# Performance work log

Measured on AMD Instinct MI355X. Metric: run time of the kernel, lower is better.

Reference implementation:

```python
import jax, jax.numpy as jnp
import numpy as np

N_NODES = 50000
N_EDGES = 800000
IN_CH, HIDDEN, OUT_CH = 128, 128, 64
EPS = 1e-5


def setup_inputs() -> dict:
    key = jax.random.key(0)
    ks = jax.random.split(key, 16)
    s = lambda fan_in: 1.0 / np.sqrt(fan_in)
    return {
        "x": jax.random.normal(ks[0], (N_NODES, IN_CH), dtype=jnp.float32),
        "edge_index": jax.random.randint(ks[1], (2, N_EDGES), 0, N_NODES, dtype=jnp.int64),
        # SAGEConv1: lin_l (neighbors, with bias), lin_r (root, no bias)
        "Wl1": jax.random.uniform(ks[2], (HIDDEN, IN_CH), jnp.float32, -s(IN_CH), s(IN_CH)),
        "bl1": jnp.zeros((HIDDEN,), jnp.float32),
        "Wr1": jax.random.uniform(ks[3], (HIDDEN, IN_CH), jnp.float32, -s(IN_CH), s(IN_CH)),
        # SAGEConv2
        "Wl2": jax.random.uniform(ks[4], (HIDDEN, HIDDEN), jnp.float32, -s(HIDDEN), s(HIDDEN)),
        "bl2": jnp.zeros((HIDDEN,), jnp.float32),
        "Wr2": jax.random.uniform(ks[5], (HIDDEN, HIDDEN), jnp.float32, -s(HIDDEN), s(HIDDEN)),
        # SAGEConv3
        "Wl3": jax.random.uniform(ks[6], (OUT_CH, HIDDEN), jnp.float32, -s(HIDDEN), s(HIDDEN)),
        "bl3": jnp.zeros((OUT_CH,), jnp.float32),
        "Wr3": jax.random.uniform(ks[7], (OUT_CH, HIDDEN), jnp.float32, -s(HIDDEN), s(HIDDEN)),
        # LayerNorms
        "g1": jnp.ones((HIDDEN,), jnp.float32),
        "beta1": jnp.zeros((HIDDEN,), jnp.float32),
        "g2": jnp.ones((HIDDEN,), jnp.float32),
        "beta2": jnp.zeros((HIDDEN,), jnp.float32),
    }


def _sage_conv(x, src, dst, n_nodes, Wl, bl, Wr):
    # mean aggregation of source features at target nodes (PyG SAGEConv, aggr='mean')
    msg = x[src]                                             # [E, C] gather
    sums = jax.ops.segment_sum(msg, dst, num_segments=n_nodes)
    cnt = jax.ops.segment_sum(jnp.ones((src.shape[0],), x.dtype), dst, num_segments=n_nodes)
    mean = sums / jnp.maximum(cnt, 1.0)[:, None]
    return mean @ Wl.T + bl + x @ Wr.T


def _layernorm(h, g, b):
    mu = jnp.mean(h, axis=-1, keepdims=True)
    var = jnp.mean(jnp.square(h - mu), axis=-1, keepdims=True)
    return (h - mu) * jax.lax.rsqrt(var + EPS) * g + b


def reference(x, edge_index, Wl1, bl1, Wr1, Wl2, bl2, Wr2, Wl3, bl3, Wr3, g1, beta1, g2, beta2):
    src, dst = edge_index[0], edge_index[1]
    n = x.shape[0]
    h = jax.nn.relu(_sage_conv(x, src, dst, n, Wl1, bl1, Wr1))
    h = _layernorm(h, g1, beta1)
    h = jax.nn.relu(_sage_conv(h, src, dst, n, Wl2, bl2, Wr2))
    h = _layernorm(h, g2, beta2)
    return _sage_conv(h, src, dst, n, Wl3, bl3, Wr3)
```

## Files before the change

kernel.cpp:

```cpp
#include <hip/hip_runtime.h>

#define NNODES 50000
#define NEDGES 800000
#define FILL_CHUNK 7168
#define FILL_NCHUNK 112
#define FILL_BLOCKS (FILL_NCHUNK * 8)
#define GEMM_BLOCKS ((NNODES + 127) / 128)
#define FUSE_BLOCKS ((NNODES + 127) / 128)
#define CAP 64
#define HSTRIDE 136

using bf16x8  = __attribute__((ext_vector_type(8))) __bf16;
using floatx4 = __attribute__((ext_vector_type(4))) float;

__device__ __forceinline__ float bf2f(unsigned short u) {
  unsigned int v = ((unsigned int)u) << 16;
  return __builtin_bit_cast(float, v);
}
__device__ __forceinline__ unsigned short f2bf(float f) {
  unsigned int u = __builtin_bit_cast(unsigned int, f);
  u += 0x7fffu + ((u >> 16) & 1u);
  return (unsigned short)(u >> 16);
}

__device__ __forceinline__ signed char enc_i8(float f) {
  float g = fminf(fmaxf(f * 32.0f, -127.0f), 127.0f);
  return (signed char)__float2int_rn(g);
}

struct WPtrs {
  const float* src[6];
  unsigned short* dst[6];
  int n[6];
};

__global__ __launch_bounds__(256) void convw_zero_kernel(WPtrs p, int* __restrict__ cnt) {
  if (blockIdx.x < 320) {
    int i = blockIdx.x * 256 + threadIdx.x;
#pragma unroll
    for (int s = 0; s < 6; ++s) {
      if (i < p.n[s]) {
        p.dst[s][i] = f2bf(p.src[s][i]);
        return;
      }
      i -= p.n[s];
    }
  } else {
    int i = (blockIdx.x - 320) * 256 + threadIdx.x;
    if (i < NNODES) cnt[i] = 0;
  }
}

__device__ __forceinline__ void fill_body(int bid, const int* __restrict__ src,
                                          const int* __restrict__ dst,
                                          int* __restrict__ cnt,
                                          int* __restrict__ bucket) {
  int p = bid & 7;
  if (p == 7) return;
  int chunk = bid >> 3;
  int e0 = chunk * FILL_CHUNK;
  int e1 = min(e0 + FILL_CHUNK, NEDGES);
  for (int base = e0 + (int)threadIdx.x * 4; base < e1; base += 256 * 4) {
    int4 d4 = *(const int4*)(dst + base);
    int4 s4 = *(const int4*)(src + base);
    if ((d4.x >> 13) == p) { int sl = atomicAdd(&cnt[d4.x], 1); if (sl < CAP) bucket[(size_t)d4.x * CAP + sl] = s4.x; }
    if ((d4.y >> 13) == p) { int sl = atomicAdd(&cnt[d4.y], 1); if (sl < CAP) bucket[(size_t)d4.y * CAP + sl] = s4.y; }
    if ((d4.z >> 13) == p) { int sl = atomicAdd(&cnt[d4.z], 1); if (sl < CAP) bucket[(size_t)d4.z * CAP + sl] = s4.z; }
    if ((d4.w >> 13) == p) { int sl = atomicAdd(&cnt[d4.w], 1); if (sl < CAP) bucket[(size_t)d4.w * CAP + sl] = s4.w; }
  }
}

__device__ __forceinline__ bf16x8 load_frag(const unsigned short* p) {
  uint4 v = *(const uint4*)p;
  return __builtin_bit_cast(bf16x8, v);
}
__device__ __forceinline__ bf16x8 cvt_frag(const float* p) {
  float4 v0 = *(const float4*)p;
  float4 v1 = *(const float4*)(p + 4);
  uint4 o;
  o.x = (unsigned int)f2bf(v0.x) | ((unsigned int)f2bf(v0.y) << 16);
  o.y = (unsigned int)f2bf(v0.z) | ((unsigned int)f2bf(v0.w) << 16);
  o.z = (unsigned int)f2bf(v1.x) | ((unsigned int)f2bf(v1.y) << 16);
  o.w = (unsigned int)f2bf(v1.z) | ((unsigned int)f2bf(v1.w) << 16);
  return __builtin_bit_cast(bf16x8, o);
}

template <int NTL, int NTR, bool F32IN>
__device__ __forceinline__ void gemm_dual_body(int bid, const void* __restrict__ Ain,
                                               const unsigned short* __restrict__ W,
                                               signed char* __restrict__ yl,
                                               unsigned short* __restrict__ yr) {
  constexpr int NT = NTL + NTR;
  int wave = threadIdx.x >> 6;
  int lane = threadIdx.x & 63;
  int quad = lane >> 4;
  int m = lane & 15;
  int row0 = bid * 128 + wave * 32;
  int ar0 = min(row0 + m, NNODES - 1);
  int ar1 = min(row0 + 16 + m, NNODES - 1);
  bf16x8 a0[4], a1[4];
#pragma unroll
  for (int kt = 0; kt < 4; ++kt) {
    if constexpr (F32IN) {
      const float* A = (const float*)Ain;
      a0[kt] = cvt_frag(A + (size_t)ar0 * 128 + quad * 8 + kt * 32);
      a1[kt] = cvt_frag(A + (size_t)ar1 * 128 + quad * 8 + kt * 32);
    } else {
      const unsigned short* A = (const unsigned short*)Ain;
      a0[kt] = load_frag(A + (size_t)ar0 * 128 + quad * 8 + kt * 32);
      a1[kt] = load_frag(A + (size_t)ar1 * 128 + quad * 8 + kt * 32);
    }
  }
#pragma unroll
  for (int t = 0; t < NT; ++t) {
    const unsigned short* wp = W + (t * 16 + m) * 128 + quad * 8;
    bf16x8 w[4];
#pragma unroll
    for (int kt = 0; kt < 4; ++kt) w[kt] = load_frag(wp + kt * 32);
    floatx4 c0 = {0.f, 0.f, 0.f, 0.f};
    floatx4 c1 = {0.f, 0.f, 0.f, 0.f};
#pragma unroll
    for (int kt = 0; kt < 4; ++kt) {
      c0 = __builtin_amdgcn_mfma_f32_16x16x32_bf16(a0[kt], w[kt], c0, 0, 0, 0);
      c1 = __builtin_amdgcn_mfma_f32_16x16x32_bf16(a1[kt], w[kt], c1, 0, 0, 0);
    }
#pragma unroll
    for (int r = 0; r < 4; ++r) {
      int g0 = row0 + quad * 4 + r;
      int g1r = g0 + 16;
      if (t < NTL) {
        int col = t * 16 + m;
        if (g0 < NNODES) yl[(size_t)g0 * (NTL * 16) + col] = enc_i8(c0[r]);
        if (g1r < NNODES) yl[(size_t)g1r * (NTL * 16) + col] = enc_i8(c1[r]);
      } else {
        int col = (t - NTL) * 16 + m;
        if (g0 < NNODES) yr[(size_t)g0 * (NTR * 16) + col] = f2bf(c0[r]);
        if (g1r < NNODES) yr[(size_t)g1r * (NTR * 16) + col] = f2bf(c1[r]);
      }
    }
  }
}

__global__ __launch_bounds__(256) void fill_gemm1_kernel(
    const int* __restrict__ src, const int* __restrict__ dst, int* __restrict__ cnt,
    int* __restrict__ bucket, const float* __restrict__ x,
    const unsigned short* __restrict__ W, signed char* __restrict__ yl,
    unsigned short* __restrict__ yr) {
  if (blockIdx.x < FILL_BLOCKS)
    fill_body(blockIdx.x, src, dst, cnt, bucket);
  else
    gemm_dual_body<8, 8, true>(blockIdx.x - FILL_BLOCKS, x, W, yl, yr);
}

#define ACCU(u, base)                                       \
  a[base] += (int)((signed char)((u) & 0xffu));             \
  a[base + 1] += (int)((signed char)(((u) >> 8) & 0xffu));  \
  a[base + 2] += (int)((signed char)(((u) >> 16) & 0xffu)); \
  a[base + 3] += (int)((signed char)((u) >> 24));
#define ACC16(v) ACCU((v).x, 0) ACCU((v).y, 4) ACCU((v).z, 8) ACCU((v).w, 12)

template <int NTL, int NTR>
__global__ __launch_bounds__(1024) void aggln_gemm_kernel(
    const signed char* __restrict__ yl_in, const unsigned short* __restrict__ yr_in,
    const float* __restrict__ bl, const float* __restrict__ g,
    const float* __restrict__ be, const int* __restrict__ cnt,
    const int* __restrict__ bucket, const unsigned short* __restrict__ W,
    signed char* __restrict__ yl_out, unsigned short* __restrict__ yr_out) {
  constexpr int NT = NTL + NTR;
  __shared__ unsigned short hlds[128 * HSTRIDE];
  int tid = (int)threadIdx.x;
  int lg = tid >> 3;
  int c8 = tid & 7;
  int gw = blockIdx.x * 128 + lg;
  int gwc = min(gw, NNODES - 1);
  int offc = c8 * 16;
  int deg = cnt[gwc];
  int ed = min(deg, CAP);
  const int* bk = bucket + (size_t)gwc * CAP;
  int a[16];
#pragma unroll
  for (int k = 0; k < 16; ++k) a[k] = 0;
  int e = 0;
  for (; e + 3 < ed; e += 4) {
    int i0 = bk[e], i1 = bk[e + 1], i2 = bk[e + 2], i3 = bk[e + 3];
    uint4 v0 = *(const uint4*)(yl_in + (size_t)i0 * 128 + offc);
    uint4 v1 = *(const uint4*)(yl_in + (size_t)i1 * 128 + offc);
    uint4 v2 = *(const uint4*)(yl_in + (size_t)i2 * 128 + offc);
    uint4 v3 = *(const uint4*)(yl_in + (size_t)i3 * 128 + offc);
    ACC16(v0) ACC16(v1) ACC16(v2) ACC16(v3)
  }
  if (e + 1 < ed) {
    int i0 = bk[e], i1 = bk[e + 1];
    uint4 v0 = *(const uint4*)(yl_in + (size_t)i0 * 128 + offc);
    uint4 v1 = *(const uint4*)(yl_in + (size_t)i1 * 128 + offc);
    ACC16(v0) ACC16(v1)
    e += 2;
  }
  if (e < ed) {
    int i0 = bk[e];
    uint4 v = *(const uint4*)(yl_in + (size_t)i0 * 128 + offc);
    ACC16(v)
  }
  float idg = 0.03125f / (float)((deg > 0) ? deg : 1);
  const unsigned short* yrp = yr_in + (size_t)gwc * 128 + offc;
  uint4 r0 = *(const uint4*)yrp;
  uint4 r1 = *(const uint4*)(yrp + 8);
  unsigned rw[8] = {r0.x, r0.y, r0.z, r0.w, r1.x, r1.y, r1.z, r1.w};
  float blv[16];
#pragma unroll
  for (int k = 0; k < 4; ++k)
    *(float4*)&blv[k * 4] = *(const float4*)(bl + offc + k * 4);
  float x[16], sA = 0.f, sB = 0.f;
#pragma unroll
  for (int k = 0; k < 16; ++k) {
    float rv = bf2f((unsigned short)((rw[k >> 1] >> ((k & 1) * 16)) & 0xffffu));
    float xv = (float)a[k] * idg + rv + blv[k];
    xv = fmaxf(xv, 0.f);
    x[k] = xv;
    sA += xv;
    sB += xv * xv;
  }
#pragma unroll
  for (int msk = 1; msk < 8; msk <<= 1) {
    sA += __shfl_xor(sA, msk, 8);
    sB += __shfl_xor(sB, msk, 8);
  }
  float mu = sA * (1.0f / 128.0f);
  float var = sB * (1.0f / 128.0f) - mu * mu;
  float rs = rsqrtf(var + 1e-5f);
  float gv[16], bev[16];
#pragma unroll
  for (int k = 0; k < 4; ++k) {
    *(float4*)&gv[k * 4] = *(const float4*)(g + offc + k * 4);
    *(float4*)&bev[k * 4] = *(const float4*)(be + offc + k * 4);
  }
  unsigned ow[8];
#pragma unroll
  for (int k = 0; k < 8; ++k) {
    float y0 = (x[2 * k] - mu) * rs * gv[2 * k] + bev[2 * k];
    float y1 = (x[2 * k + 1] - mu) * rs * gv[2 * k + 1] + bev[2 * k + 1];
    ow[k] = (unsigned)f2bf(y0) | ((unsigned)f2bf(y1) << 16);
  }
  uint4* hp = (uint4*)&hlds[lg * HSTRIDE + offc];
  hp[0] = make_uint4(ow[0], ow[1], ow[2], ow[3]);
  hp[1] = make_uint4(ow[4], ow[5], ow[6], ow[7]);
  __syncthreads();
  int wave = tid >> 6;
  if (wave >= 8) return;
  int lane = tid & 63;
  int quad = lane >> 4;
  int m = lane & 15;
  int row0 = blockIdx.x * 128 + wave * 16;
  int lr = wave * 16 + m;
  bf16x8 a0[4];
#pragma unroll
  for (int kt = 0; kt < 4; ++kt)
    a0[kt] = load_frag(&hlds[lr * HSTRIDE + quad * 8 + kt * 32]);
#pragma unroll
  for (int t = 0; t < NT; ++t) {
    const unsigned short* wp = W + (t * 16 + m) * 128 + quad * 8;
    bf16x8 w[4];
#pragma unroll
    for (int kt = 0; kt < 4; ++kt) w[kt] = load_frag(wp + kt * 32);
    floatx4 c0 = {0.f, 0.f, 0.f, 0.f};
#pragma unroll
    for (int kt = 0; kt < 4; ++kt)
      c0 = __builtin_amdgcn_mfma_f32_16x16x32_bf16(a0[kt], w[kt], c0, 0, 0, 0);
#pragma unroll
    for (int r = 0; r < 4; ++r) {
      int g0 = row0 + quad * 4 + r;
      if (g0 < NNODES) {
        if (t < NTL)
          yl_out[(size_t)g0 * (NTL * 16) + t * 16 + m] = enc_i8(c0[r]);
        else
          yr_out[(size_t)g0 * (NTR * 16) + (t - NTL) * 16 + m] = f2bf(c0[r]);
      }
    }
  }
}

__global__ __launch_bounds__(256) void agg3_kernel(
    const signed char* __restrict__ yl, const unsigned short* __restrict__ yr,
    const float* __restrict__ bl, const int* __restrict__ cnt,
    const int* __restrict__ bucket, float* __restrict__ out) {
  int wid = (blockIdx.x * blockDim.x + threadIdx.x) >> 6;
  int lane = threadIdx.x & 63;
  int grp = lane >> 2;
  int c4 = lane & 3;
  int gw = wid * 16 + grp;
  if (gw >= NNODES) return;
  int offc = c4 * 16;
  int deg = cnt[gw];
  int ed = min(deg, CAP);
  const int* bk = bucket + (size_t)gw * CAP;
  int a[16];
#pragma unroll
  for (int k = 0; k < 16; ++k) a[k] = 0;
  int e = 0;
  for (; e + 3 < ed; e += 4) {
    int i0 = bk[e], i1 = bk[e + 1], i2 = bk[e + 2], i3 = bk[e + 3];
    uint4 v0 = *(const uint4*)(yl + (size_t)i0 * 64 + offc);
    uint4 v1 = *(const uint4*)(yl + (size_t)i1 * 64 + offc);
    uint4 v2 = *(const uint4*)(yl + (size_t)i2 * 64 + offc);
    uint4 v3 = *(const uint4*)(yl + (size_t)i3 * 64 + offc);
    ACC16(v0) ACC16(v1) ACC16(v2) ACC16(v3)
  }
  if (e + 1 < ed) {
    int i0 = bk[e], i1 = bk[e + 1];
    uint4 v0 = *(const uint4*)(yl + (size_t)i0 * 64 + offc);
    uint4 v1 = *(const uint4*)(yl + (size_t)i1 * 64 + offc);
    ACC16(v0) ACC16(v1)
    e += 2;
  }
  if (e < ed) {
    int i0 = bk[e];
    uint4 v = *(const uint4*)(yl + (size_t)i0 * 64 + offc);
    ACC16(v)
  }
  float idg = 0.03125f / (float)((deg > 0) ? deg : 1);
  const unsigned short* yrp = yr + (size_t)gw * 64 + offc;
  uint4 r0 = *(const uint4*)yrp;
  uint4 r1 = *(const uint4*)(yrp + 8);
  unsigned rw[8] = {r0.x, r0.y, r0.z, r0.w, r1.x, r1.y, r1.z, r1.w};
  float blv[16];
#pragma unroll
  for (int k = 0; k < 4; ++k)
    *(float4*)&blv[k * 4] = *(const float4*)(bl + offc + k * 4);
  float o[16];
#pragma unroll
  for (int k = 0; k < 16; ++k) {
    float rv = bf2f((unsigned short)((rw[k >> 1] >> ((k & 1) * 16)) & 0xffffu));
    o[k] = (float)a[k] * idg + rv + blv[k];
  }
  float* op = out + (size_t)gw * 64 + offc;
#pragma unroll
  for (int k = 0; k < 4; ++k) *(float4*)(op + k * 4) = *(float4*)&o[k * 4];
}

extern "C" void kernel_launch(void* const* d_in, const int* in_sizes, int n_in,
                              void* d_out, int out_size, void* d_ws, size_t ws_size,
                              hipStream_t stream) {
  const float* x = (const float*)d_in[0];
  const int* ei = (const int*)d_in[1];
  const int* srcv = ei;
  const int* dstv = ei + NEDGES;
  const float* Wl1 = (const float*)d_in[2];
  const float* bl1 = (const float*)d_in[3];
  const float* Wr1 = (const float*)d_in[4];
  const float* Wl2 = (const float*)d_in[5];
  const float* bl2 = (const float*)d_in[6];
  const float* Wr2 = (const float*)d_in[7];
  const float* Wl3 = (const float*)d_in[8];
  const float* bl3 = (const float*)d_in[9];
  const float* Wr3 = (const float*)d_in[10];
  const float* g1 = (const float*)d_in[11];
  const float* be1 = (const float*)d_in[12];
  const float* g2 = (const float*)d_in[13];
  const float* be2 = (const float*)d_in[14];

  char* ws = (char*)d_ws;
  size_t o = 0;
  int* cnt = (int*)(ws + o);      o += 200192;
  int* bucket = (int*)(ws + o);   o += (size_t)NNODES * CAP * 4;
  unsigned short* wb1 = (unsigned short*)(ws + o); o += 65536;
  unsigned short* wb2 = (unsigned short*)(ws + o); o += 65536;
  unsigned short* wb3 = (unsigned short*)(ws + o); o += 32768;
  signed char* yl1 = (signed char*)(ws + o);       o += (size_t)50000 * 128;
  unsigned short* yr1 = (unsigned short*)(ws + o); o += (size_t)50000 * 256;
  signed char* yl2 = (signed char*)(ws + o);       o += (size_t)50000 * 128;
  unsigned short* yr2 = (unsigned short*)(ws + o); o += (size_t)50000 * 256;
  signed char* yl3 = (signed char*)(ws + o);       o += (size_t)50000 * 64;
  unsigned short* yr3 = (unsigned short*)(ws + o); o += (size_t)50000 * 128;

  dim3 blk(256);
  dim3 fblk(1024);
  dim3 agg3Grid((NNODES + 63) / 64);

  WPtrs wp;
  wp.src[0] = Wl1; wp.dst[0] = wb1;         wp.n[0] = 128 * 128;
  wp.src[1] = Wr1; wp.dst[1] = wb1 + 16384; wp.n[1] = 128 * 128;
  wp.src[2] = Wl2; wp.dst[2] = wb2;         wp.n[2] = 128 * 128;
  wp.src[3] = Wr2; wp.dst[3] = wb2 + 16384; wp.n[3] = 128 * 128;
  wp.src[4] = Wl3; wp.dst[4] = wb3;         wp.n[4] = 64 * 128;
  wp.src[5] = Wr3; wp.dst[5] = wb3 + 8192;  wp.n[5] = 64 * 128;

  convw_zero_kernel<<<dim3(320 + 196), blk, 0, stream>>>(wp, cnt);
  fill_gemm1_kernel<<<dim3(FILL_BLOCKS + GEMM_BLOCKS), blk, 0, stream>>>(
      srcv, dstv, cnt, bucket, x, wb1, yl1, yr1);
  aggln_gemm_kernel<8, 8><<<dim3(FUSE_BLOCKS), fblk, 0, stream>>>(
      yl1, yr1, bl1, g1, be1, cnt, bucket, wb2, yl2, yr2);
  aggln_gemm_kernel<4, 4><<<dim3(FUSE_BLOCKS), fblk, 0, stream>>>(
      yl2, yr2, bl2, g2, be2, cnt, bucket, wb3, yl3, yr3);
  agg3_kernel<<<agg3Grid, blk, 0, stream>>>(yl3, yr3, bl3, cnt, bucket, (float*)d_out);
}
```

Baseline: 264.6 us.

## Shrink fused aggregate-LN-GEMM blocks to 32 rows, all waves sharing MFMA work

The fused aggregation+LayerNorm+GEMM kernel now uses 256-thread blocks covering 32 nodes instead of 1024-thread blocks covering 128 nodes. The MFMA stage is restructured so all four waves split the output column tiles and each computes two 16-row tiles, where before only 8 of 16 waves did GEMM work and the rest exited. This aims to raise occupancy and scheduling flexibility and to stop idling half the block during the GEMM. In exchange, each weight tile is now reloaded by four times as many blocks, raising global/L2 traffic for the weights. The gamma/beta loads are also hoisted earlier.

```diff
diff --git a/kernel.cpp b/kernel.cpp
--- a/kernel.cpp
+++ b/kernel.cpp
@@ -6,7 +6,7 @@
 #define FILL_NCHUNK 112
 #define FILL_BLOCKS (FILL_NCHUNK * 8)
 #define GEMM_BLOCKS ((NNODES + 127) / 128)
-#define FUSE_BLOCKS ((NNODES + 127) / 128)
+#define FUSE_BLOCKS ((NNODES + 31) / 32)
 #define CAP 64
 #define HSTRIDE 136
 
@@ -160,18 +160,19 @@
 #define ACC16(v) ACCU((v).x, 0) ACCU((v).y, 4) ACCU((v).z, 8) ACCU((v).w, 12)
 
 template <int NTL, int NTR>
-__global__ __launch_bounds__(1024) void aggln_gemm_kernel(
+__global__ __launch_bounds__(256) void aggln_gemm32_kernel(
     const signed char* __restrict__ yl_in, const unsigned short* __restrict__ yr_in,
     const float* __restrict__ bl, const float* __restrict__ g,
     const float* __restrict__ be, const int* __restrict__ cnt,
     const int* __restrict__ bucket, const unsigned short* __restrict__ W,
     signed char* __restrict__ yl_out, unsigned short* __restrict__ yr_out) {
   constexpr int NT = NTL + NTR;
-  __shared__ unsigned short hlds[128 * HSTRIDE];
+  constexpr int TPW = NT / 4;
+  __shared__ unsigned short hlds[32 * HSTRIDE];
   int tid = (int)threadIdx.x;
   int lg = tid >> 3;
   int c8 = tid & 7;
-  int gw = blockIdx.x * 128 + lg;
+  int gw = blockIdx.x * 32 + lg;
   int gwc = min(gw, NNODES - 1);
   int offc = c8 * 16;
   int deg = cnt[gwc];
@@ -206,10 +207,13 @@
   uint4 r0 = *(const uint4*)yrp;
   uint4 r1 = *(const uint4*)(yrp + 8);
   unsigned rw[8] = {r0.x, r0.y, r0.z, r0.w, r1.x, r1.y, r1.z, r1.w};
-  float blv[16];
-#pragma unroll
-  for (int k = 0; k < 4; ++k)
+  float blv[16], gv[16], bev[16];
+#pragma unroll
+  for (int k = 0; k < 4; ++k) {
     *(float4*)&blv[k * 4] = *(const float4*)(bl + offc + k * 4);
+    *(float4*)&gv[k * 4] = *(const float4*)(g + offc + k * 4);
+    *(float4*)&bev[k * 4] = *(const float4*)(be + offc + k * 4);
+  }
   float x[16], sA = 0.f, sB = 0.f;
 #pragma unroll
   for (int k = 0; k < 16; ++k) {
@@ -228,12 +232,6 @@
   float mu = sA * (1.0f / 128.0f);
   float var = sB * (1.0f / 128.0f) - mu * mu;
   float rs = rsqrtf(var + 1e-5f);
-  float gv[16], bev[16];
-#pragma unroll
-  for (int k = 0; k < 4; ++k) {
-    *(float4*)&gv[k * 4] = *(const float4*)(g + offc + k * 4);
-    *(float4*)&bev[k * 4] = *(const float4*)(be + offc + k * 4);
-  }
   unsigned ow[8];
 #pragma unroll
   for (int k = 0; k < 8; ++k) {
@@ -246,34 +244,42 @@
   hp[1] = make_uint4(ow[4], ow[5], ow[6], ow[7]);
   __syncthreads();
   int wave = tid >> 6;
-  if (wave >= 8) return;
   int lane = tid & 63;
   int quad = lane >> 4;
   int m = lane & 15;
-  int row0 = blockIdx.x * 128 + wave * 16;
-  int lr = wave * 16 + m;
-  bf16x8 a0[4];
-#pragma unroll
-  for (int kt = 0; kt < 4; ++kt)
-    a0[kt] = load_frag(&hlds[lr * HSTRIDE + quad * 8 + kt * 32]);
-#pragma unroll
-  for (int t = 0; t < NT; ++t) {
+  int row0 = blockIdx.x * 32;
+  bf16x8 a0[4], a1[4];
+#pragma unroll
+  for (int kt = 0; kt < 4; ++kt) {
+    a0[kt] = load_frag(&hlds[m * HSTRIDE + quad * 8 + kt * 32]);
+    a1[kt] = load_frag(&hlds[(16 + m) * HSTRIDE + quad * 8 + kt * 32]);
+  }
+#pragma unroll
+  for (int tt = 0; tt < TPW; ++tt) {
+    int t = wave * TPW + tt;
     const unsigned short* wp = W + (t * 16 + m) * 128 + quad * 8;
     bf16x8 w[4];
 #pragma unroll
     for (int kt = 0; kt < 4; ++kt) w[kt] = load_frag(wp + kt * 32);
     floatx4 c0 = {0.f, 0.f, 0.f, 0.f};
-#pragma unroll
-    for (int kt = 0; kt < 4; ++kt)
+    floatx4 c1 = {0.f, 0.f, 0.f, 0.f};
+#pragma unroll
+    for (int kt = 0; kt < 4; ++kt) {
       c0 = __builtin_amdgcn_mfma_f32_16x16x32_bf16(a0[kt], w[kt], c0, 0, 0, 0);
+      c1 = __builtin_amdgcn_mfma_f32_16x16x32_bf16(a1[kt], w[kt], c1, 0, 0, 0);
+    }
 #pragma unroll
     for (int r = 0; r < 4; ++r) {
       int g0 = row0 + quad * 4 + r;
-      if (g0 < NNODES) {
-        if (t < NTL)
-          yl_out[(size_t)g0 * (NTL * 16) + t * 16 + m] = enc_i8(c0[r]);
-        else
-          yr_out[(size_t)g0 * (NTR * 16) + (t - NTL) * 16 + m] = f2bf(c0[r]);
+      int g1r = g0 + 16;
+      if (t < NTL) {
+        int col = t * 16 + m;
+        if (g0 < NNODES) yl_out[(size_t)g0 * (NTL * 16) + col] = enc_i8(c0[r]);
+        if (g1r < NNODES) yl_out[(size_t)g1r * (NTL * 16) + col] = enc_i8(c1[r]);
+      } else {
+        int col = (t - NTL) * 16 + m;
+        if (g0 < NNODES) yr_out[(size_t)g0 * (NTR * 16) + col] = f2bf(c0[r]);
+        if (g1r < NNODES) yr_out[(size_t)g1r * (NTR * 16) + col] = f2bf(c1[r]);
       }
     }
   }
@@ -373,7 +379,7 @@
   unsigned short* yr3 = (unsigned short*)(ws + o); o += (size_t)50000 * 128;
 
   dim3 blk(256);
-  dim3 fblk(1024);
+  dim3 fuseGrid(FUSE_BLOCKS);
   dim3 agg3Grid((NNODES + 63) / 64);
 
   WPtrs wp;
@@ -387,9 +393,9 @@
   convw_zero_kernel<<<dim3(320 + 196), blk, 0, stream>>>(wp, cnt);
   fill_gemm1_kernel<<<dim3(FILL_BLOCKS + GEMM_BLOCKS), blk, 0, stream>>>(
       srcv, dstv, cnt, bucket, x, wb1, yl1, yr1);
-  aggln_gemm_kernel<8, 8><<<dim3(FUSE_BLOCKS), fblk, 0, stream>>>(
+  aggln_gemm32_kernel<8, 8><<<fuseGrid, blk, 0, stream>>>(
       yl1, yr1, bl1, g1, be1, cnt, bucket, wb2, yl2, yr2);
-  aggln_gemm_kernel<4, 4><<<dim3(FUSE_BLOCKS), fblk, 0, stream>>>(
+  aggln_gemm32_kernel<4, 4><<<fuseGrid, blk, 0, stream>>>(
       yl2, yr2, bl2, g2, be2, cnt, bucket, wb3, yl3, yr3);
   agg3_kernel<<<agg3Grid, blk, 0, stream>>>(yl3, yr3, bl3, cnt, bucket, (float*)d_out);
 }
```

Result: faster. 232.8 us (-12.0%).
